# Kernel tuning notes

Measured on AMD Instinct MI355X. Metric: run time of the kernel, lower is better.

## Reference

```python
import jax, jax.numpy as jnp
import numpy as np
from jax import lax

DN = ('NCHW', 'OIHW', 'NCHW')
EPS = 1e-9
MASK_THR = 1e-3


def box_filter(x, size):
    # Separable box (ones) filter with SAME padding; x: [1,1,H,W]
    pad = size // 2
    kv = jnp.ones((1, 1, size, 1), x.dtype)
    kh = jnp.ones((1, 1, 1, size), x.dtype)
    y = lax.conv_general_dilated(x, kv, (1, 1), [(pad, pad), (0, 0)], dimension_numbers=DN)
    return lax.conv_general_dilated(y, kh, (1, 1), [(0, 0), (pad, pad)], dimension_numbers=DN)


def setup_inputs() -> dict:
    key = jax.random.key(0)
    k1, k2, k3, k4 = jax.random.split(key, 4)
    H = W = 2048
    I = jax.random.uniform(k1, (1, 1, H, W), jnp.float32)            # image in [0,1]
    u = jax.random.uniform(k2, (1, 4, H, W), jnp.float32)            # class memberships
    b = 1.0 + 0.1 * jax.random.normal(k3, (1, 1, H, W), jnp.float32)  # bias field ~1
    e = jax.random.normal(k4, (1, 1, H, W), jnp.float32) * 0.1       # residual
    return {"I": I, "u": u, "b": b, "e": e, "p": 2, "size": 21}


def reference(I, u, b, e, p, size):
    C = u.shape[1]
    e_d = lax.stop_gradient(e)
    b_d = lax.stop_gradient(b)
    up = u ** p                      # [1,C,H,W]
    b2 = b_d * b_d
    mask = (I > MASK_THR).astype(I.dtype)
    norm = box_filter(mask, size)    # partialFilter: local valid-pixel count

    def filt(x):                     # convParFilt: mask-normalized local mean
        return box_filter(x, size) / (norm + EPS)

    b_K = filt(b)
    b2_K = filt(b2)

    # classCenter (vectorized over classes 1..C-1)
    A = (I - e_d) * b_K                                   # [1,1,H,W]
    num = jnp.sum(A * up[:, 1:], axis=(0, 2, 3))          # [C-1]
    den = jnp.sum(b2_K * up[:, 1:], axis=(0, 2, 3))       # [C-1]
    c0 = jnp.sum(I * up[:, :1]) / (jnp.sum(up[:, :1]) + EPS)
    v = jnp.concatenate([c0[None], num / (den + EPS)])    # [C]

    # bias-field update: convolution is linear, so sum over classes first
    vb = v[None, :, None, None]
    bd = filt((I - e_d) * jnp.sum(vb * up, axis=1, keepdims=True))
    db = filt(jnp.sum(vb * vb * up, axis=1, keepdims=True))
    bd = bd * mask + (1.0 - mask)
    db = db * mask + (1.0 - mask)
    b_new = bd / (db + EPS)
    diff = b - b_new
    return jnp.mean(diff * diff)
```

## Files before the change

kernel.cpp:

```cpp
#include <hip/hip_runtime.h>

constexpr int Hh = 2048;
constexpr int Ww = 2048;
constexpr int NN = Hh * Ww;
constexpr int W4 = Ww / 4;
constexpr int NN4 = NN / 4;
constexpr int RAD = 10;
constexpr float EPSf = 1e-9f;
constexpr float MASK_THRf = 0.001f;
constexpr int SEGW = 58;
constexpr int NSEG = 9;
constexpr int BH = 8;
constexpr int NBAND = Hh / BH;
constexpr int NWAVE = NSEG * NBAND;

__device__ inline float rcpf(float x) { return __builtin_amdgcn_rcpf(x); }

__device__ inline float waveReduce(float v) {
    #pragma unroll
    for (int o = 32; o > 0; o >>= 1) v += __shfl_down(v, o, 64);
    return v;
}

__device__ inline float4 f4zero() { float4 z; z.x = z.y = z.z = z.w = 0.f; return z; }

__device__ inline float4 hbox(float4 v, int lane) {
    float S = v.x + v.y + v.z + v.w;
    float Sm2 = __shfl(S, lane - 2, 64);
    float Sm1 = __shfl(S, lane - 1, 64);
    float Sp1 = __shfl(S, lane + 1, 64);
    float Sp2 = __shfl(S, lane + 2, 64);
    float T5 = Sm2 + Sm1 + S + Sp1 + Sp2;
    float wm3 = __shfl(v.w, lane - 3, 64);
    float zm3 = __shfl(v.z, lane - 3, 64);
    float xm2 = __shfl(v.x, lane - 2, 64);
    float wp2 = __shfl(v.w, lane + 2, 64);
    float xp3 = __shfl(v.x, lane + 3, 64);
    float yp3 = __shfl(v.y, lane + 3, 64);
    float4 r;
    r.y = T5 + wm3;
    r.z = T5 + xp3;
    r.x = r.y + zm3 - wp2;
    r.w = r.z + yp3 - xm2;
    return r;
}

__device__ inline void winA(float4& sm, float4& sb, float4& sq,
                            float4 iv, float4 bv, float f) {
    sm.x += f * ((iv.x > MASK_THRf) ? 1.f : 0.f);
    sm.y += f * ((iv.y > MASK_THRf) ? 1.f : 0.f);
    sm.z += f * ((iv.z > MASK_THRf) ? 1.f : 0.f);
    sm.w += f * ((iv.w > MASK_THRf) ? 1.f : 0.f);
    sb.x += f * bv.x; sb.y += f * bv.y; sb.z += f * bv.z; sb.w += f * bv.w;
    sq.x += f * (bv.x * bv.x); sq.y += f * (bv.y * bv.y);
    sq.z += f * (bv.z * bv.z); sq.w += f * (bv.w * bv.w);
}

__device__ inline void winB(float4& sp, float4& sq, float4& sm,
                            float4 pv, float4 qv, float4 iv, float f) {
    sp.x += f * pv.x; sp.y += f * pv.y; sp.z += f * pv.z; sp.w += f * pv.w;
    sq.x += f * qv.x; sq.y += f * qv.y; sq.z += f * qv.z; sq.w += f * qv.w;
    sm.x += f * ((iv.x > MASK_THRf) ? 1.f : 0.f);
    sm.y += f * ((iv.y > MASK_THRf) ? 1.f : 0.f);
    sm.z += f * ((iv.z > MASK_THRf) ? 1.f : 0.f);
    sm.w += f * ((iv.w > MASK_THRf) ? 1.f : 0.f);
}

__device__ inline void k2_pix(float bm, float bb, float bb2, float Iv, float ev,
                              float u0, float u1, float u2, float u3, float* a) {
    float rn = rcpf(bm + EPSf);
    float bK = bb * rn;
    float b2K = bb2 * rn;
    float p0 = u0 * u0, p1 = u1 * u1, p2 = u2 * u2, p3 = u3 * u3;
    a[0] += Iv * p0;
    a[1] += p0;
    float A = (Iv - ev) * bK;
    a[2] += A * p1; a[3] += A * p2; a[4] += A * p3;
    a[5] += b2K * p1; a[6] += b2K * p2; a[7] += b2K * p3;
}

__global__ __launch_bounds__(64, 2) void kA(
        const float* __restrict__ I, const float* __restrict__ B,
        const float* __restrict__ E, const float* __restrict__ U,
        float* __restrict__ partA) {
    int lane = threadIdx.x;
    int wid = blockIdx.x;
    int strip = wid % NSEG;
    int band = wid / NSEG;
    int xc = strip * SEGW - 3 + lane;
    bool inb = (unsigned)xc < (unsigned)W4;
    int xl = inb ? xc : 0;
    int y0 = band * BH;

    const float4* I4 = (const float4*)I;
    const float4* B4 = (const float4*)B;
    const float4* E4 = (const float4*)E;
    const float4* U0 = (const float4*)U;
    const float4* U1 = U0 + NN4;
    const float4* U2 = U1 + NN4;
    const float4* U3 = U2 + NN4;

    float4 sm = f4zero(), sb = f4zero(), sq = f4zero();
    #pragma unroll
    for (int k = 0; k < 2 * RAD + 1; ++k) {
        int r = y0 - RAD - 1 + k;
        float f = ((unsigned)r < (unsigned)Hh) ? 1.f : 0.f;
        int rc = (r < 0) ? 0 : ((r > Hh - 1) ? Hh - 1 : r);
        winA(sm, sb, sq, I4[rc * W4 + xl], B4[rc * W4 + xl], f);
    }

    float a[8] = {0, 0, 0, 0, 0, 0, 0, 0};
    #pragma unroll 1
    for (int yy = 0; yy < BH; yy += 2) {
        int y = y0 + yy;
        int hd0 = y + RAD, hd1 = y + RAD + 1;
        int tl0 = y - RAD - 1, tl1 = y - RAD;
        float fh0 = (hd0 < Hh) ? 1.f : 0.f;
        float fh1 = (hd1 < Hh) ? 1.f : 0.f;
        float ft0 = (tl0 >= 0) ? -1.f : 0.f;
        float ft1 = (tl1 >= 0) ? -1.f : 0.f;
        int rh0 = (hd0 < Hh) ? hd0 : Hh - 1;
        int rh1 = (hd1 < Hh) ? hd1 : Hh - 1;
        int rt0 = (tl0 >= 0) ? tl0 : 0;
        int rt1 = (tl1 >= 0) ? tl1 : 0;
        float4 ih0 = I4[rh0 * W4 + xl], bh0 = B4[rh0 * W4 + xl];
        float4 ih1 = I4[rh1 * W4 + xl], bh1 = B4[rh1 * W4 + xl];
        float4 it0 = I4[rt0 * W4 + xl], bt0 = B4[rt0 * W4 + xl];
        float4 it1 = I4[rt1 * W4 + xl], bt1 = B4[rt1 * W4 + xl];
        int xo0 = y * W4 + xl, xo1 = (y + 1) * W4 + xl;
        float4 Iv0 = I4[xo0], Ev0 = E4[xo0];
        float4 u00 = U0[xo0], u10 = U1[xo0], u20 = U2[xo0], u30 = U3[xo0];
        float4 Iv1 = I4[xo1], Ev1 = E4[xo1];
        float4 u01 = U0[xo1], u11 = U1[xo1], u21 = U2[xo1], u31 = U3[xo1];
        winA(sm, sb, sq, ih0, bh0, fh0);
        winA(sm, sb, sq, it0, bt0, ft0);
        {
            float4 vm = inb ? sm : f4zero();
            float4 vb = inb ? sb : f4zero();
            float4 vq = inb ? sq : f4zero();
            float4 bm = hbox(vm, lane);
            float4 bb = hbox(vb, lane);
            float4 bq = hbox(vq, lane);
            if (inb && lane >= 3 && lane <= 60) {
                k2_pix(bm.x, bb.x, bq.x, Iv0.x, Ev0.x, u00.x, u10.x, u20.x, u30.x, a);
                k2_pix(bm.y, bb.y, bq.y, Iv0.y, Ev0.y, u00.y, u10.y, u20.y, u30.y, a);
                k2_pix(bm.z, bb.z, bq.z, Iv0.z, Ev0.z, u00.z, u10.z, u20.z, u30.z, a);
                k2_pix(bm.w, bb.w, bq.w, Iv0.w, Ev0.w, u00.w, u10.w, u20.w, u30.w, a);
            }
        }
        winA(sm, sb, sq, ih1, bh1, fh1);
        winA(sm, sb, sq, it1, bt1, ft1);
        {
            float4 vm = inb ? sm : f4zero();
            float4 vb = inb ? sb : f4zero();
            float4 vq = inb ? sq : f4zero();
            float4 bm = hbox(vm, lane);
            float4 bb = hbox(vb, lane);
            float4 bq = hbox(vq, lane);
            if (inb && lane >= 3 && lane <= 60) {
                k2_pix(bm.x, bb.x, bq.x, Iv1.x, Ev1.x, u01.x, u11.x, u21.x, u31.x, a);
                k2_pix(bm.y, bb.y, bq.y, Iv1.y, Ev1.y, u01.y, u11.y, u21.y, u31.y, a);
                k2_pix(bm.z, bb.z, bq.z, Iv1.z, Ev1.z, u01.z, u11.z, u21.z, u31.z, a);
                k2_pix(bm.w, bb.w, bq.w, Iv1.w, Ev1.w, u01.w, u11.w, u21.w, u31.w, a);
            }
        }
    }

    #pragma unroll
    for (int k = 0; k < 8; ++k) a[k] = waveReduce(a[k]);
    if (lane == 0) {
        float4 r0, r1;
        r0.x = a[0]; r0.y = a[1]; r0.z = a[2]; r0.w = a[3];
        r1.x = a[4]; r1.y = a[5]; r1.z = a[6]; r1.w = a[7];
        ((float4*)partA)[wid * 2]     = r0;
        ((float4*)partA)[wid * 2 + 1] = r1;
    }
}

__global__ __launch_bounds__(1024) void k3_v(const float* __restrict__ partA, float* __restrict__ vV) {
    __shared__ float s[1024];
    int tid = threadIdx.x;
    float acc = 0.f;
    #pragma unroll
    for (int j = 0; j < (NWAVE * 8) / 1024; ++j) acc += partA[tid + j * 1024];
    s[tid] = acc;
    __syncthreads();
    #pragma unroll
    for (int st = 512; st >= 8; st >>= 1) {
        if (tid < st) s[tid] += s[tid + st];
        __syncthreads();
    }
    if (tid == 0) {
        vV[0] = s[0] / (s[1] + EPSf);
        vV[1] = s[2] / (s[5] + EPSf);
        vV[2] = s[3] / (s[6] + EPSf);
        vV[3] = s[4] / (s[7] + EPSf);
    }
}

__global__ __launch_bounds__(256) void kP(
        const float* __restrict__ I, const float* __restrict__ E, const float* __restrict__ U,
        const float* __restrict__ vV,
        float* __restrict__ P, float* __restrict__ Q) {
    int idx = blockIdx.x * 256 + threadIdx.x;
    float v0 = vV[0], v1 = vV[1], v2 = vV[2], v3 = vV[3];
    float w0 = v0 * v0, w1 = v1 * v1, w2 = v2 * v2, w3 = v3 * v3;
    const float4* I4 = (const float4*)I;
    const float4* E4 = (const float4*)E;
    const float4* U0 = (const float4*)U;
    const float4* U1 = U0 + NN4;
    const float4* U2 = U1 + NN4;
    const float4* U3 = U2 + NN4;
    float4 Iv = I4[idx], Ev = E4[idx];
    float4 a0 = U0[idx], a1 = U1[idx], a2 = U2[idx], a3 = U3[idx];
    float4 p, q;
    float p0, p1, p2, p3;
    p0 = a0.x * a0.x; p1 = a1.x * a1.x; p2 = a2.x * a2.x; p3 = a3.x * a3.x;
    p.x = (Iv.x - Ev.x) * (v0 * p0 + v1 * p1 + v2 * p2 + v3 * p3);
    q.x = w0 * p0 + w1 * p1 + w2 * p2 + w3 * p3;
    p0 = a0.y * a0.y; p1 = a1.y * a1.y; p2 = a2.y * a2.y; p3 = a3.y * a3.y;
    p.y = (Iv.y - Ev.y) * (v0 * p0 + v1 * p1 + v2 * p2 + v3 * p3);
    q.y = w0 * p0 + w1 * p1 + w2 * p2 + w3 * p3;
    p0 = a0.z * a0.z; p1 = a1.z * a1.z; p2 = a2.z * a2.z; p3 = a3.z * a3.z;
    p.z = (Iv.z - Ev.z) * (v0 * p0 + v1 * p1 + v2 * p2 + v3 * p3);
    q.z = w0 * p0 + w1 * p1 + w2 * p2 + w3 * p3;
    p0 = a0.w * a0.w; p1 = a1.w * a1.w; p2 = a2.w * a2.w; p3 = a3.w * a3.w;
    p.w = (Iv.w - Ev.w) * (v0 * p0 + v1 * p1 + v2 * p2 + v3 * p3);
    q.w = w0 * p0 + w1 * p1 + w2 * p2 + w3 * p3;
    ((float4*)P)[idx] = p;
    ((float4*)Q)[idx] = q;
}

__global__ __launch_bounds__(64, 2) void kB(
        const float* __restrict__ P, const float* __restrict__ Q,
        const float* __restrict__ I, const float* __restrict__ B,
        float* __restrict__ partL) {
    int lane = threadIdx.x;
    int wid = blockIdx.x;
    int strip = wid % NSEG;
    int band = wid / NSEG;
    int xc = strip * SEGW - 3 + lane;
    bool inb = (unsigned)xc < (unsigned)W4;
    int xl = inb ? xc : 0;
    int y0 = band * BH;

    const float4* P4 = (const float4*)P;
    const float4* Q4 = (const float4*)Q;
    const float4* I4 = (const float4*)I;
    const float4* B4 = (const float4*)B;

    float4 sp = f4zero(), sqq = f4zero(), sm = f4zero();
    #pragma unroll
    for (int k = 0; k < 2 * RAD + 1; ++k) {
        int r = y0 - RAD - 1 + k;
        float f = ((unsigned)r < (unsigned)Hh) ? 1.f : 0.f;
        int rc = (r < 0) ? 0 : ((r > Hh - 1) ? Hh - 1 : r);
        winB(sp, sqq, sm, P4[rc * W4 + xl], Q4[rc * W4 + xl], I4[rc * W4 + xl], f);
    }

    float a = 0.f;
    #pragma unroll 1
    for (int yy = 0; yy < BH; yy += 2) {
        int y = y0 + yy;
        int hd0 = y + RAD, hd1 = y + RAD + 1;
        int tl0 = y - RAD - 1, tl1 = y - RAD;
        float fh0 = (hd0 < Hh) ? 1.f : 0.f;
        float fh1 = (hd1 < Hh) ? 1.f : 0.f;
        float ft0 = (tl0 >= 0) ? -1.f : 0.f;
        float ft1 = (tl1 >= 0) ? -1.f : 0.f;
        int rh0 = (hd0 < Hh) ? hd0 : Hh - 1;
        int rh1 = (hd1 < Hh) ? hd1 : Hh - 1;
        int rt0 = (tl0 >= 0) ? tl0 : 0;
        int rt1 = (tl1 >= 0) ? tl1 : 0;
        float4 ph0 = P4[rh0 * W4 + xl], qh0 = Q4[rh0 * W4 + xl], mh0 = I4[rh0 * W4 + xl];
        float4 ph1 = P4[rh1 * W4 + xl], qh1 = Q4[rh1 * W4 + xl], mh1 = I4[rh1 * W4 + xl];
        float4 pt0 = P4[rt0 * W4 + xl], qt0 = Q4[rt0 * W4 + xl], mt0 = I4[rt0 * W4 + xl];
        float4 pt1 = P4[rt1 * W4 + xl], qt1 = Q4[rt1 * W4 + xl], mt1 = I4[rt1 * W4 + xl];
        int xo0 = y * W4 + xl, xo1 = (y + 1) * W4 + xl;
        float4 Iv0 = I4[xo0], Bv0 = B4[xo0];
        float4 Iv1 = I4[xo1], Bv1 = B4[xo1];
        winB(sp, sqq, sm, ph0, qh0, mh0, fh0);
        winB(sp, sqq, sm, pt0, qt0, mt0, ft0);
        {
            float4 vP = inb ? sp : f4zero();
            float4 vQ = inb ? sqq : f4zero();
            float4 vM = inb ? sm : f4zero();
            float4 bP = hbox(vP, lane);
            float4 bQ = hbox(vQ, lane);
            float4 bM = hbox(vM, lane);
            if (inb && lane >= 3 && lane <= 60) {
                {
                    float rn = rcpf(bM.x + EPSf);
                    float bd = bP.x * rn, db = bQ.x * rn;
                    float m = (Iv0.x > MASK_THRf) ? 1.f : 0.f;
                    bd = bd * m + (1.f - m); db = db * m + (1.f - m);
                    float d = Bv0.x - bd * rcpf(db + EPSf); a += d * d;
                }
                {
                    float rn = rcpf(bM.y + EPSf);
                    float bd = bP.y * rn, db = bQ.y * rn;
                    float m = (Iv0.y > MASK_THRf) ? 1.f : 0.f;
                    bd = bd * m + (1.f - m); db = db * m + (1.f - m);
                    float d = Bv0.y - bd * rcpf(db + EPSf); a += d * d;
                }
                {
                    float rn = rcpf(bM.z + EPSf);
                    float bd = bP.z * rn, db = bQ.z * rn;
                    float m = (Iv0.z > MASK_THRf) ? 1.f : 0.f;
                    bd = bd * m + (1.f - m); db = db * m + (1.f - m);
                    float d = Bv0.z - bd * rcpf(db + EPSf); a += d * d;
                }
                {
                    float rn = rcpf(bM.w + EPSf);
                    float bd = bP.w * rn, db = bQ.w * rn;
                    float m = (Iv0.w > MASK_THRf) ? 1.f : 0.f;
                    bd = bd * m + (1.f - m); db = db * m + (1.f - m);
                    float d = Bv0.w - bd * rcpf(db + EPSf); a += d * d;
                }
            }
        }
        winB(sp, sqq, sm, ph1, qh1, mh1, fh1);
        winB(sp, sqq, sm, pt1, qt1, mt1, ft1);
        {
            float4 vP = inb ? sp : f4zero();
            float4 vQ = inb ? sqq : f4zero();
            float4 vM = inb ? sm : f4zero();
            float4 bP = hbox(vP, lane);
            float4 bQ = hbox(vQ, lane);
            float4 bM = hbox(vM, lane);
            if (inb && lane >= 3 && lane <= 60) {
                {
                    float rn = rcpf(bM.x + EPSf);
                    float bd = bP.x * rn, db = bQ.x * rn;
                    float m = (Iv1.x > MASK_THRf) ? 1.f : 0.f;
                    bd = bd * m + (1.f - m); db = db * m + (1.f - m);
                    float d = Bv1.x - bd * rcpf(db + EPSf); a += d * d;
                }
                {
                    float rn = rcpf(bM.y + EPSf);
                    float bd = bP.y * rn, db = bQ.y * rn;
                    float m = (Iv1.y > MASK_THRf) ? 1.f : 0.f;
                    bd = bd * m + (1.f - m); db = db * m + (1.f - m);
                    float d = Bv1.y - bd * rcpf(db + EPSf); a += d * d;
                }
                {
                    float rn = rcpf(bM.z + EPSf);
                    float bd = bP.z * rn, db = bQ.z * rn;
                    float m = (Iv1.z > MASK_THRf) ? 1.f : 0.f;
                    bd = bd * m + (1.f - m); db = db * m + (1.f - m);
                    float d = Bv1.z - bd * rcpf(db + EPSf); a += d * d;
                }
                {
                    float rn = rcpf(bM.w + EPSf);
                    float bd = bP.w * rn, db = bQ.w * rn;
                    float m = (Iv1.w > MASK_THRf) ? 1.f : 0.f;
                    bd = bd * m + (1.f - m); db = db * m + (1.f - m);
                    float d = Bv1.w - bd * rcpf(db + EPSf); a += d * d;
                }
            }
        }
    }

    a = waveReduce(a);
    if (lane == 0) partL[wid] = a;
}

__global__ __launch_bounds__(1024) void k6_out(const float* __restrict__ partL, float* __restrict__ out) {
    __shared__ float s[1024];
    int tid = threadIdx.x;
    float acc = 0.f;
    for (int c = tid; c < NWAVE; c += 1024) acc += partL[c];
    s[tid] = acc;
    __syncthreads();
    #pragma unroll
    for (int st = 512; st >= 1; st >>= 1) {
        if (tid < st) s[tid] += s[tid + st];
        __syncthreads();
    }
    if (tid == 0) out[0] = s[0] / (float)NN;
}

extern "C" void kernel_launch(void* const* d_in, const int* in_sizes, int n_in,
                              void* d_out, int out_size, void* d_ws, size_t ws_size,
                              hipStream_t stream) {
    const float* I = (const float*)d_in[0];
    const float* U = (const float*)d_in[1];
    const float* B = (const float*)d_in[2];
    const float* E = (const float*)d_in[3];

    float* P     = (float*)d_ws;
    float* Q     = P + NN;
    float* partA = Q + NN;
    float* partL = partA + NWAVE * 8;
    float* vV    = partL + NWAVE;

    kA<<<NWAVE, 64, 0, stream>>>(I, B, E, U, partA);
    k3_v<<<1, 1024, 0, stream>>>(partA, vV);
    kP<<<NN4 / 256, 256, 0, stream>>>(I, E, U, vV, P, Q);
    kB<<<NWAVE, 64, 0, stream>>>(P, Q, I, B, partL);
    k6_out<<<1, 1024, 0, stream>>>(partL, (float*)d_out);
}
```

Measured before the change: 225.6 us.

## Group three strip waves per block and swizzle blocks across XCDs

The two stencil-reduction kernels now run three adjacent column-strip waves per 192-thread block instead of one wave per block. Block indices are remapped so that consecutive logical blocks, which are neighbouring row bands, land on the same XCD. The goal is to improve L2 reuse of the overlapping halo rows between bands and to cut per-block launch overhead. This assumes blocks are dispatched round-robin across 8 XCDs, and larger blocks may reduce scheduling flexibility.

```diff
diff --git a/kernel.cpp b/kernel.cpp
--- a/kernel.cpp
+++ b/kernel.cpp
@@ -13,6 +13,11 @@
 constexpr int BH = 8;
 constexpr int NBAND = Hh / BH;
 constexpr int NWAVE = NSEG * NBAND;
+constexpr int WPB = 3;
+constexpr int SPB = NSEG / WPB;
+constexpr int NBLK = NBAND * SPB;
+constexpr int NXCD = 8;
+constexpr int CPX = NBLK / NXCD;
 
 __device__ inline float rcpf(float x) { return __builtin_amdgcn_rcpf(x); }
 
@@ -79,14 +84,19 @@
     a[5] += b2K * p1; a[6] += b2K * p2; a[7] += b2K * p3;
 }
 
-__global__ __launch_bounds__(64, 2) void kA(
+__device__ inline int xcdSwz(int b) { return (b % NXCD) * CPX + b / NXCD; }
+
+__global__ __launch_bounds__(192, 2) void kA(
         const float* __restrict__ I, const float* __restrict__ B,
         const float* __restrict__ E, const float* __restrict__ U,
         float* __restrict__ partA) {
-    int lane = threadIdx.x;
-    int wid = blockIdx.x;
-    int strip = wid % NSEG;
-    int band = wid / NSEG;
+    int lane = threadIdx.x & 63;
+    int wave = threadIdx.x >> 6;
+    int orig = xcdSwz(blockIdx.x);
+    int band = orig / SPB;
+    int sb = orig - band * SPB;
+    int strip = sb * WPB + wave;
+    int wid = orig * WPB + wave;
     int xc = strip * SEGW - 3 + lane;
     bool inb = (unsigned)xc < (unsigned)W4;
     int xl = inb ? xc : 0;
@@ -100,13 +110,13 @@
     const float4* U2 = U1 + NN4;
     const float4* U3 = U2 + NN4;
 
-    float4 sm = f4zero(), sb = f4zero(), sq = f4zero();
+    float4 sm = f4zero(), sb4 = f4zero(), sq = f4zero();
     #pragma unroll
     for (int k = 0; k < 2 * RAD + 1; ++k) {
         int r = y0 - RAD - 1 + k;
         float f = ((unsigned)r < (unsigned)Hh) ? 1.f : 0.f;
         int rc = (r < 0) ? 0 : ((r > Hh - 1) ? Hh - 1 : r);
-        winA(sm, sb, sq, I4[rc * W4 + xl], B4[rc * W4 + xl], f);
+        winA(sm, sb4, sq, I4[rc * W4 + xl], B4[rc * W4 + xl], f);
     }
 
     float a[8] = {0, 0, 0, 0, 0, 0, 0, 0};
@@ -132,11 +142,11 @@
         float4 u00 = U0[xo0], u10 = U1[xo0], u20 = U2[xo0], u30 = U3[xo0];
         float4 Iv1 = I4[xo1], Ev1 = E4[xo1];
         float4 u01 = U0[xo1], u11 = U1[xo1], u21 = U2[xo1], u31 = U3[xo1];
-        winA(sm, sb, sq, ih0, bh0, fh0);
-        winA(sm, sb, sq, it0, bt0, ft0);
+        winA(sm, sb4, sq, ih0, bh0, fh0);
+        winA(sm, sb4, sq, it0, bt0, ft0);
         {
             float4 vm = inb ? sm : f4zero();
-            float4 vb = inb ? sb : f4zero();
+            float4 vb = inb ? sb4 : f4zero();
             float4 vq = inb ? sq : f4zero();
             float4 bm = hbox(vm, lane);
             float4 bb = hbox(vb, lane);
@@ -148,11 +158,11 @@
                 k2_pix(bm.w, bb.w, bq.w, Iv0.w, Ev0.w, u00.w, u10.w, u20.w, u30.w, a);
             }
         }
-        winA(sm, sb, sq, ih1, bh1, fh1);
-        winA(sm, sb, sq, it1, bt1, ft1);
+        winA(sm, sb4, sq, ih1, bh1, fh1);
+        winA(sm, sb4, sq, it1, bt1, ft1);
         {
             float4 vm = inb ? sm : f4zero();
-            float4 vb = inb ? sb : f4zero();
+            float4 vb = inb ? sb4 : f4zero();
             float4 vq = inb ? sq : f4zero();
             float4 bm = hbox(vm, lane);
             float4 bb = hbox(vb, lane);
@@ -231,14 +241,17 @@
     ((float4*)Q)[idx] = q;
 }
 
-__global__ __launch_bounds__(64, 2) void kB(
+__global__ __launch_bounds__(192, 2) void kB(
         const float* __restrict__ P, const float* __restrict__ Q,
         const float* __restrict__ I, const float* __restrict__ B,
         float* __restrict__ partL) {
-    int lane = threadIdx.x;
-    int wid = blockIdx.x;
-    int strip = wid % NSEG;
-    int band = wid / NSEG;
+    int lane = threadIdx.x & 63;
+    int wave = threadIdx.x >> 6;
+    int orig = xcdSwz(blockIdx.x);
+    int band = orig / SPB;
+    int sb = orig - band * SPB;
+    int strip = sb * WPB + wave;
+    int wid = orig * WPB + wave;
     int xc = strip * SEGW - 3 + lane;
     bool inb = (unsigned)xc < (unsigned)W4;
     int xl = inb ? xc : 0;
@@ -394,9 +407,9 @@
     float* partL = partA + NWAVE * 8;
     float* vV    = partL + NWAVE;
 
-    kA<<<NWAVE, 64, 0, stream>>>(I, B, E, U, partA);
+    kA<<<NBLK, 192, 0, stream>>>(I, B, E, U, partA);
     k3_v<<<1, 1024, 0, stream>>>(partA, vV);
     kP<<<NN4 / 256, 256, 0, stream>>>(I, E, U, vV, P, Q);
-    kB<<<NWAVE, 64, 0, stream>>>(P, Q, I, B, partL);
+    kB<<<NBLK, 192, 0, stream>>>(P, Q, I, B, partL);
     k6_out<<<1, 1024, 0, stream>>>(partL, (float*)d_out);
 }
```

Result: faster. 199.6 us (-11.5%).
